# Kernel optimization log

Measured on AMD Instinct MI355X. Metric: run time of the kernel, lower is better.

The kernel has to match this reference:

```python
import jax, jax.numpy as jnp
import numpy as np

C = 256      # channels
G = 8        # groups
Cg = C // G  # channels per group (32, %16==0)
KS = 3       # kernel_size
PAD = 1
STRIDE = 1
DIL = 1
OS = 1.0     # offset_scale
DW = 3       # dw_kernel_size
Kg = KS * KS                      # sample points per group (remove_center=0)
D_OM = int(np.ceil(G * Kg * 3 / 8) * 8)  # 216, offset_mask linear out dim
N, H, W = 16, 56, 56


def setup_inputs() -> dict:
    key = jax.random.key(0)
    ks = jax.random.split(key, 8)
    inp = {}
    inp['ref'] = jax.random.normal(ks[0], (N, C, H, W), jnp.float32)
    inp['input'] = jax.random.normal(ks[1], (N, C, H, W), jnp.float32)
    inp['value_w'] = jax.random.normal(ks[2], (C, C), jnp.float32) * (1.0 / np.sqrt(C))
    inp['value_b'] = jnp.zeros((C,), jnp.float32)
    inp['dw_w'] = jax.random.normal(ks[3], (C, 2, DW, DW), jnp.float32) * 0.1
    inp['dw_b'] = jnp.zeros((C,), jnp.float32)
    # original zero-inits offset_mask; use small random weights so sampling is non-trivial
    inp['om_w'] = jax.random.normal(ks[4], (D_OM, C), jnp.float32) * 0.02
    inp['om_b'] = jnp.zeros((D_OM,), jnp.float32)
    inp['out_w'] = jax.random.normal(ks[5], (C, C), jnp.float32) * (1.0 / np.sqrt(C))
    inp['out_b'] = jnp.zeros((C,), jnp.float32)
    return inp


def _dcnv4(ref, inp, value_w, value_b, dw_w, dw_b, om_w, om_b, out_w, out_b):
    n, _, h, w = inp.shape
    # value projection on tokens (N, HW, C)
    tokens = inp.reshape(n, C, h * w).transpose(0, 2, 1)
    xv = (tokens @ value_w.T + value_b).reshape(n, h, w, G, Cg)
    # grouped depthwise-style conv on concat([input, ref]) -> offset/mask features
    cat = jnp.concatenate([inp, ref], axis=1)  # (N, 2C, H, W)
    dw = jax.lax.conv_general_dilated(
        cat, dw_w, (1, 1), ((DW // 2, DW // 2), (DW // 2, DW // 2)),
        dimension_numbers=('NCHW', 'OIHW', 'NCHW'), feature_group_count=C)
    dw = dw + dw_b[None, :, None, None]
    om = dw.transpose(0, 2, 3, 1) @ om_w.T + om_b            # (N,H,W,D_OM)
    om = om[..., :G * Kg * 3].reshape(n, h, w, G, Kg * 3)    # drop pad cols (none here)
    off = om[..., :2 * Kg].reshape(n, h, w, G, Kg, 2)        # (dx, dy) per point
    mask = om[..., 2 * Kg:]                                  # (N,H,W,G,Kg), DCNv4: no softmax
    # sampling locations (index coords): h*stride - pad + i*dil + os*dy
    ii, jj = jnp.meshgrid(jnp.arange(KS), jnp.arange(KS), indexing='ij')
    gy = (ii.reshape(-1) * DIL - PAD).astype(inp.dtype)      # (Kg,)
    gx = (jj.reshape(-1) * DIL - PAD).astype(inp.dtype)
    hh = (jnp.arange(h, dtype=inp.dtype) * STRIDE)[None, :, None, None, None]
    ww = (jnp.arange(w, dtype=inp.dtype) * STRIDE)[None, None, :, None, None]
    iy = hh + gy + OS * off[..., 1]                          # (N,H,W,G,Kg)
    ix = ww + gx + OS * off[..., 0]
    # bilinear sample with zero padding, mask-weighted sum over points
    y0 = jnp.floor(iy); x0 = jnp.floor(ix)
    fy = iy - y0; fx = ix - x0
    y0i = y0.astype(jnp.int32); x0i = x0.astype(jnp.int32)
    nidx = jnp.arange(n)[:, None, None, None, None]
    gidx = jnp.arange(G)[None, None, None, :, None]
    out = jnp.zeros((n, h, w, G, Cg), inp.dtype)
    for dy in (0, 1):
        for dx in (0, 1):
            yy = y0i + dy; xx = x0i + dx
            wgt = (fy if dy else 1.0 - fy) * (fx if dx else 1.0 - fx)
            valid = (yy >= 0) & (yy < h) & (xx >= 0) & (xx < w)
            yyc = jnp.clip(yy, 0, h - 1); xxc = jnp.clip(xx, 0, w - 1)
            gathered = xv[nidx, yyc, xxc, gidx]              # (N,H,W,G,Kg,Cg)
            out = out + jnp.einsum('nhwgp,nhwgpc->nhwgc', wgt * valid * mask, gathered)
    y = out.reshape(n, h * w, C) @ out_w.T + out_b
    return y.transpose(0, 2, 1).reshape(n, C, h, w)


def reference(ref, input, value_w, value_b, dw_w, dw_b, om_w, om_b, out_w, out_b):
    return _dcnv4(ref, input, value_w, value_b, dw_w, dw_b, om_w, om_b, out_w, out_b)
```

## Files before the change

kernel.cpp:

```cpp
#include <hip/hip_runtime.h>

#define HW 3136
#define WID 56
#define HEI 56
#define NCH 256
#define NB 16
#define MTOT (NB * HW)

typedef __attribute__((ext_vector_type(8))) short bf16x8;
typedef __attribute__((ext_vector_type(8))) unsigned short u16x8;
typedef __attribute__((ext_vector_type(4))) float f32x4;

__device__ __forceinline__ unsigned int f2bf(float f) {
    unsigned int x = __float_as_uint(f);
    return (x + 0x7fffu + ((x >> 16) & 1u)) >> 16;
}
__device__ __forceinline__ float bf2f(unsigned short u) {
    return __uint_as_float(((unsigned int)u) << 16);
}

__global__ __launch_bounds__(256) void cvt_weights(const float* __restrict__ vw,
                                                   const float* __restrict__ ow,
                                                   const float* __restrict__ outw,
                                                   unsigned short* __restrict__ dvw,
                                                   unsigned short* __restrict__ dow,
                                                   unsigned short* __restrict__ doutw) {
    int i = blockIdx.x * 256 + threadIdx.x;
    if (i < 65536) dvw[i] = (unsigned short)f2bf(vw[i]);
    else if (i < 120832) dow[i - 65536] = (unsigned short)f2bf(ow[i - 65536]);
    else if (i < 186368) doutw[i - 120832] = (unsigned short)f2bf(outw[i - 120832]);
}

template <int DOUT, int A_MODE, int OUT_MODE>
__global__ __launch_bounds__(256) void gemm_kernel(const void* __restrict__ Aptr,
                                                   const unsigned short* __restrict__ Bw,
                                                   const float* __restrict__ bias,
                                                   void* __restrict__ Out) {
    int bid = blockIdx.x;
    int nt = bid & 1;
    int mt = bid >> 1;
    int p0 = mt * 128;
    int tid = threadIdx.x;
    int lane = tid & 63;
    int wv = tid >> 6;
    int wm = wv & 1, wn = wv >> 1;
    int n0 = nt * 128;

    __shared__ __align__(16) char lds[16384 + 16384];
    char* As = lds;
    char* Bs = lds + 16384;

    int l15 = lane & 15;
    int l4 = lane >> 4;

    f32x4 acc[4][4];
    #pragma unroll
    for (int nf = 0; nf < 4; ++nf) {
        int ch = n0 + wn * 64 + nf * 16 + l15;
        float bv = (ch < DOUT) ? bias[ch] : 0.f;
        #pragma unroll
        for (int mf = 0; mf < 4; ++mf) acc[mf][nf] = (f32x4){bv, bv, bv, bv};
    }

    for (int t = 0; t < 4; ++t) {
        int k0 = t * 64;
        if (A_MODE == 0 || A_MODE == 1) {
            int px = tid & 127, kh = tid >> 7;
            unsigned int gpix = p0 + px;
            unsigned int n = gpix / HW;
            unsigned int rem = gpix - n * HW;
            #pragma unroll
            for (int h = 0; h < 4; ++h) {
                u16x8 v;
                if (A_MODE == 0) {
                    const float* src = (const float*)Aptr + ((size_t)(n * 256 + k0 + kh * 32 + h * 8)) * HW + rem;
                    #pragma unroll
                    for (int j = 0; j < 8; ++j) v[j] = (unsigned short)f2bf(src[(size_t)j * HW]);
                } else {
                    const unsigned short* src = (const unsigned short*)Aptr + ((size_t)(n * 256 + k0 + kh * 32 + h * 8)) * HW + rem;
                    #pragma unroll
                    for (int j = 0; j < 8; ++j) v[j] = src[(size_t)j * HW];
                }
                int byte = (px * 128 + (kh * 32 + h * 8) * 2) ^ ((px & 7) << 4);
                *(u16x8*)(As + byte) = v;
            }
        } else {
            int row = tid >> 1, q = tid & 1;
            const unsigned short* src = (const unsigned short*)Aptr + (size_t)(p0 + row) * 256 + k0 + q * 32;
            #pragma unroll
            for (int h = 0; h < 4; ++h) {
                u16x8 v = *(const u16x8*)(src + h * 8);
                int byte = (row * 128 + (q * 32 + h * 8) * 2) ^ ((row & 7) << 4);
                *(u16x8*)(As + byte) = v;
            }
        }
        {
            int bch = tid >> 1, kh = tid & 1;
            int ch = n0 + bch;
            bool valid = (ch < DOUT);
            const unsigned short* src = Bw + (size_t)ch * 256 + k0 + kh * 32;
            #pragma unroll
            for (int q = 0; q < 4; ++q) {
                u16x8 v = (u16x8){0, 0, 0, 0, 0, 0, 0, 0};
                if (valid) v = *(const u16x8*)(src + q * 8);
                int byte = (bch * 128 + (kh * 32 + q * 8) * 2) ^ ((bch & 7) << 4);
                *(u16x8*)(Bs + byte) = v;
            }
        }
        __syncthreads();
        bf16x8 af[4][2], bfr[4][2];
        #pragma unroll
        for (int mf = 0; mf < 4; ++mf)
            #pragma unroll
            for (int kf = 0; kf < 2; ++kf) {
                int row = wm * 64 + mf * 16 + l15;
                int byte = (row * 128 + (kf * 32 + l4 * 8) * 2) ^ ((row & 7) << 4);
                af[mf][kf] = *(bf16x8*)(As + byte);
            }
        #pragma unroll
        for (int nf = 0; nf < 4; ++nf)
            #pragma unroll
            for (int kf = 0; kf < 2; ++kf) {
                int row = wn * 64 + nf * 16 + l15;
                int byte = (row * 128 + (kf * 32 + l4 * 8) * 2) ^ ((row & 7) << 4);
                bfr[nf][kf] = *(bf16x8*)(Bs + byte);
            }
        #pragma unroll
        for (int mf = 0; mf < 4; ++mf)
            #pragma unroll
            for (int nf = 0; nf < 4; ++nf)
                #pragma unroll
                for (int kf = 0; kf < 2; ++kf)
                    acc[mf][nf] = __builtin_amdgcn_mfma_f32_16x16x32_bf16(af[mf][kf], bfr[nf][kf], acc[mf][nf], 0, 0, 0);
        __syncthreads();
    }

    #pragma unroll
    for (int mf = 0; mf < 4; ++mf) {
        int pxb = wm * 64 + mf * 16 + l4 * 4;
        unsigned int gpix = p0 + pxb;
        #pragma unroll
        for (int nf = 0; nf < 4; ++nf) {
            int ch = n0 + wn * 64 + nf * 16 + l15;
            if (OUT_MODE == 0) {
                if (ch < DOUT) {
                    float* o = (float*)Out + (size_t)gpix * DOUT + ch;
                    #pragma unroll
                    for (int j = 0; j < 4; ++j) o[(size_t)j * DOUT] = acc[mf][nf][j];
                }
            } else if (OUT_MODE == 1) {
                if (ch < DOUT) {
                    unsigned short* o = (unsigned short*)Out + (size_t)gpix * DOUT + ch;
                    #pragma unroll
                    for (int j = 0; j < 4; ++j) o[(size_t)j * DOUT] = (unsigned short)f2bf(acc[mf][nf][j]);
                }
            } else {
                unsigned int n = gpix / HW;
                unsigned int rem = gpix - n * HW;
                float* o = (float*)Out + ((size_t)(n * 256 + ch)) * HW + rem;
                *(f32x4*)o = acc[mf][nf];
            }
        }
    }
}

__global__ __launch_bounds__(256) void dwconv_kernel(const float* __restrict__ input,
                                                     const float* __restrict__ ref,
                                                     const float* __restrict__ dw_w,
                                                     const float* __restrict__ dw_b,
                                                     unsigned short* __restrict__ out) {
    int blk = blockIdx.x;
    int yt = blk % 14;
    int cb = (blk / 14) & 63;
    int n = blk / (14 * 64);
    int tid = threadIdx.x;
    int x = tid & 63;
    int c = cb * 4 + (tid >> 6);
    int y0 = yt * 4;

    const float* src = (c < 128) ? input : ref;
    int ch0 = (c < 128) ? (2 * c) : (2 * c - 256);

    float w[18];
    #pragma unroll
    for (int i = 0; i < 18; ++i) w[i] = dw_w[c * 18 + i];

    if (x < WID) {
        float bv = dw_b[c];
        float acc[4] = {bv, bv, bv, bv};
        #pragma unroll
        for (int ch = 0; ch < 2; ++ch) {
            const float* base = src + (size_t)(n * NCH + ch0 + ch) * HW;
            #pragma unroll
            for (int r = 0; r < 6; ++r) {
                int yy = y0 - 1 + r;
                bool vy = (yy >= 0) && (yy < HEI);
                const float* row = base + yy * WID;
                float lt = (vy && x > 0) ? row[x - 1] : 0.f;
                float md = vy ? row[x] : 0.f;
                float rt = (vy && x < WID - 1) ? row[x + 1] : 0.f;
                #pragma unroll
                for (int o = 0; o < 4; ++o) {
                    int ky = r - o;
                    if (ky >= 0 && ky < 3) {
                        acc[o] += lt * w[ch * 9 + ky * 3 + 0] + md * w[ch * 9 + ky * 3 + 1] + rt * w[ch * 9 + ky * 3 + 2];
                    }
                }
            }
        }
        unsigned short* o = out + (size_t)(n * NCH + c) * HW + y0 * WID + x;
        #pragma unroll
        for (int j = 0; j < 4; ++j) o[j * WID] = (unsigned short)f2bf(acc[j]);
    }
}

__global__ __launch_bounds__(256) void sample_kernel(const float* __restrict__ xv,
                                                     const unsigned short* __restrict__ om,
                                                     unsigned short* __restrict__ sout) {
    int blk = blockIdx.x;
    int n = blk / (HW / 16);
    int p0 = (blk % (HW / 16)) * 16;
    int tid = threadIdx.x;

    __shared__ __align__(16) float swt[1152][4];
    __shared__ __align__(8) ushort soff[1152][4];

    for (int i = tid; i < 1152; i += 256) {
        int pix = i / 72;
        int r = i % 72;
        int g = r / 9;
        int pt = r % 9;
        int glob = p0 + pix;
        int py = glob / WID, px = glob % WID;
        const unsigned short* ob = om + ((size_t)n * HW + glob) * 216 + g * 27;
        float ox = bf2f(ob[2 * pt]);
        float oy = bf2f(ob[2 * pt + 1]);
        float m = bf2f(ob[18 + pt]);
        float iy = (float)(py + pt / 3 - 1) + oy;
        float ix = (float)(px + pt % 3 - 1) + ox;
        float fy0 = floorf(iy), fx0 = floorf(ix);
        float fy = iy - fy0, fx = ix - fx0;
        int y0 = (int)fy0, x0 = (int)fx0;
        #pragma unroll
        for (int dy = 0; dy < 2; ++dy) {
            #pragma unroll
            for (int dx = 0; dx < 2; ++dx) {
                int yy = y0 + dy, xx = x0 + dx;
                bool valid = (yy >= 0) & (yy < HEI) & (xx >= 0) & (xx < WID);
                int yc = min(max(yy, 0), HEI - 1);
                int xc = min(max(xx, 0), WID - 1);
                float wv = (dy ? fy : 1.f - fy) * (dx ? fx : 1.f - fx) * m;
                swt[i][dy * 2 + dx] = valid ? wv : 0.f;
                soff[i][dy * 2 + dx] = (ushort)(yc * WID + xc);
            }
        }
    }
    __syncthreads();

    int pix = tid >> 4;
    int t16 = tid & 15;
    const float* xvb = xv + (size_t)n * HW * 256;
    unsigned short* so = sout + ((size_t)n * HW + p0 + pix) * 256;

    #pragma unroll
    for (int i = 0; i < 2; ++i) {
        int chunk = t16 + 16 * i;
        int g = chunk >> 2, c8 = chunk & 3;
        int widx = pix * 72 + g * 9;
        const float* xc = xvb + g * 32 + c8 * 8;
        f32x4 a0 = (f32x4){0.f, 0.f, 0.f, 0.f};
        f32x4 a1 = (f32x4){0.f, 0.f, 0.f, 0.f};
        #pragma unroll
        for (int pt = 0; pt < 9; ++pt) {
            float4 w = *(const float4*)&swt[widx + pt][0];
            ushort4 o = *(const ushort4*)&soff[widx + pt][0];
            const float* s0 = xc + (size_t)o.x * 256;
            const float* s1 = xc + (size_t)o.y * 256;
            const float* s2 = xc + (size_t)o.z * 256;
            const float* s3 = xc + (size_t)o.w * 256;
            f32x4 w0 = (f32x4){w.x, w.x, w.x, w.x};
            f32x4 w1 = (f32x4){w.y, w.y, w.y, w.y};
            f32x4 w2 = (f32x4){w.z, w.z, w.z, w.z};
            f32x4 w3 = (f32x4){w.w, w.w, w.w, w.w};
            a0 += w0 * *(const f32x4*)(s0) + w1 * *(const f32x4*)(s1) + w2 * *(const f32x4*)(s2) + w3 * *(const f32x4*)(s3);
            a1 += w0 * *(const f32x4*)(s0 + 4) + w1 * *(const f32x4*)(s1 + 4) + w2 * *(const f32x4*)(s2 + 4) + w3 * *(const f32x4*)(s3 + 4);
        }
        u16x8 st;
        #pragma unroll
        for (int j = 0; j < 4; ++j) st[j] = (unsigned short)f2bf(a0[j]);
        #pragma unroll
        for (int j = 0; j < 4; ++j) st[4 + j] = (unsigned short)f2bf(a1[j]);
        *(u16x8*)(so + g * 32 + c8 * 8) = st;
    }
}

extern "C" void kernel_launch(void* const* d_in, const int* in_sizes, int n_in,
                              void* d_out, int out_size, void* d_ws, size_t ws_size,
                              hipStream_t stream) {
    const float* ref     = (const float*)d_in[0];
    const float* input   = (const float*)d_in[1];
    const float* value_w = (const float*)d_in[2];
    const float* value_b = (const float*)d_in[3];
    const float* dw_w    = (const float*)d_in[4];
    const float* dw_b    = (const float*)d_in[5];
    const float* om_w    = (const float*)d_in[6];
    const float* om_b    = (const float*)d_in[7];
    const float* out_w   = (const float*)d_in[8];
    const float* out_b   = (const float*)d_in[9];
    float* out = (float*)d_out;

    char* ws = (char*)d_ws;
    float* xv            = (float*)ws;
    unsigned short* dwb  = (unsigned short*)(ws + (size_t)MTOT * 256 * 4);
    unsigned short* sout = (unsigned short*)(ws + (size_t)MTOT * 256 * 6);
    unsigned short* omb  = (unsigned short*)(ws + (size_t)MTOT * 256 * 8);
    char* wbase          = ws + (size_t)MTOT * 256 * 8 + (size_t)MTOT * 216 * 2;
    unsigned short* vw_bf   = (unsigned short*)(wbase);
    unsigned short* ow_bf   = (unsigned short*)(wbase + 131072);
    unsigned short* outw_bf = (unsigned short*)(wbase + 131072 + 110592);

    cvt_weights<<<728, 256, 0, stream>>>(value_w, om_w, out_w, vw_bf, ow_bf, outw_bf);
    gemm_kernel<256, 0, 0><<<(MTOT / 128) * 2, 256, 0, stream>>>(input, vw_bf, value_b, xv);
    dwconv_kernel<<<NB * 64 * 14, 256, 0, stream>>>(input, ref, dw_w, dw_b, dwb);
    gemm_kernel<216, 1, 1><<<(MTOT / 128) * 2, 256, 0, stream>>>(dwb, ow_bf, om_b, omb);
    sample_kernel<<<NB * (HW / 16), 256, 0, stream>>>(xv, omb, sout);
    gemm_kernel<256, 2, 2><<<(MTOT / 128) * 2, 256, 0, stream>>>(sout, outw_bf, out_b, out);
}
```

Measured before the change: 330.7 us.

## Load full-K A tile once per block and store value projection in bf16

The GEMM kernel now stages the whole 128x256 A tile in LDS once and loops over both 128-column N tiles inside the block. Previously each N tile was a separate block that re-read A from global memory. The value projection output xv is now written as bf16 rather than fp32, so the sampling kernel gathers half as many bytes and converts on load. The cost is 80KB of dynamic LDS per block, which limits occupancy, plus extra bf16 rounding of the sampled values.

Measured after the change: 277.7 us. -16.0%, faster.

```diff
diff --git a/kernel.cpp b/kernel.cpp
--- a/kernel.cpp
+++ b/kernel.cpp
@@ -32,133 +32,133 @@
 }
 
 template <int DOUT, int A_MODE, int OUT_MODE>
-__global__ __launch_bounds__(256) void gemm_kernel(const void* __restrict__ Aptr,
-                                                   const unsigned short* __restrict__ Bw,
-                                                   const float* __restrict__ bias,
-                                                   void* __restrict__ Out) {
-    int bid = blockIdx.x;
-    int nt = bid & 1;
-    int mt = bid >> 1;
-    int p0 = mt * 128;
+__global__ __launch_bounds__(256, 2) void gemm_kernel(const void* __restrict__ Aptr,
+                                                      const unsigned short* __restrict__ Bw,
+                                                      const float* __restrict__ bias,
+                                                      void* __restrict__ Out) {
+    int p0 = blockIdx.x * 128;
     int tid = threadIdx.x;
     int lane = tid & 63;
     int wv = tid >> 6;
     int wm = wv & 1, wn = wv >> 1;
-    int n0 = nt * 128;
-
-    __shared__ __align__(16) char lds[16384 + 16384];
-    char* As = lds;
-    char* Bs = lds + 16384;
-
     int l15 = lane & 15;
     int l4 = lane >> 4;
 
-    f32x4 acc[4][4];
+    extern __shared__ __align__(16) char lds[];
+    char* As = lds;
+    char* Bs = lds + 65536;
+
+    if (A_MODE == 0 || A_MODE == 1) {
+        int px = tid & 127, khalf = tid >> 7;
+        unsigned int gpix = p0 + px;
+        unsigned int n = gpix / HW;
+        unsigned int rem = gpix - n * HW;
+        #pragma unroll
+        for (int h = 0; h < 16; ++h) {
+            int k = khalf * 128 + h * 8;
+            u16x8 v;
+            if (A_MODE == 0) {
+                const float* src = (const float*)Aptr + ((size_t)(n * 256 + k)) * HW + rem;
+                #pragma unroll
+                for (int j = 0; j < 8; ++j) v[j] = (unsigned short)f2bf(src[(size_t)j * HW]);
+            } else {
+                const unsigned short* src = (const unsigned short*)Aptr + ((size_t)(n * 256 + k)) * HW + rem;
+                #pragma unroll
+                for (int j = 0; j < 8; ++j) v[j] = src[(size_t)j * HW];
+            }
+            int byte = px * 512 + ((k * 2) ^ ((px & 7) << 4));
+            *(u16x8*)(As + byte) = v;
+        }
+    } else {
+        int row = tid >> 1, khalf = tid & 1;
+        const unsigned short* src = (const unsigned short*)Aptr + (size_t)(p0 + row) * 256 + khalf * 128;
+        #pragma unroll
+        for (int h = 0; h < 16; ++h) {
+            u16x8 v = *(const u16x8*)(src + h * 8);
+            int k2 = (khalf * 128 + h * 8) * 2;
+            int byte = row * 512 + (k2 ^ ((row & 7) << 4));
+            *(u16x8*)(As + byte) = v;
+        }
+    }
+
     #pragma unroll
-    for (int nf = 0; nf < 4; ++nf) {
-        int ch = n0 + wn * 64 + nf * 16 + l15;
-        float bv = (ch < DOUT) ? bias[ch] : 0.f;
-        #pragma unroll
-        for (int mf = 0; mf < 4; ++mf) acc[mf][nf] = (f32x4){bv, bv, bv, bv};
-    }
-
-    for (int t = 0; t < 4; ++t) {
-        int k0 = t * 64;
-        if (A_MODE == 0 || A_MODE == 1) {
-            int px = tid & 127, kh = tid >> 7;
-            unsigned int gpix = p0 + px;
-            unsigned int n = gpix / HW;
-            unsigned int rem = gpix - n * HW;
-            #pragma unroll
-            for (int h = 0; h < 4; ++h) {
-                u16x8 v;
-                if (A_MODE == 0) {
-                    const float* src = (const float*)Aptr + ((size_t)(n * 256 + k0 + kh * 32 + h * 8)) * HW + rem;
-                    #pragma unroll
-                    for (int j = 0; j < 8; ++j) v[j] = (unsigned short)f2bf(src[(size_t)j * HW]);
-                } else {
-                    const unsigned short* src = (const unsigned short*)Aptr + ((size_t)(n * 256 + k0 + kh * 32 + h * 8)) * HW + rem;
-                    #pragma unroll
-                    for (int j = 0; j < 8; ++j) v[j] = src[(size_t)j * HW];
-                }
-                int byte = (px * 128 + (kh * 32 + h * 8) * 2) ^ ((px & 7) << 4);
-                *(u16x8*)(As + byte) = v;
-            }
-        } else {
-            int row = tid >> 1, q = tid & 1;
-            const unsigned short* src = (const unsigned short*)Aptr + (size_t)(p0 + row) * 256 + k0 + q * 32;
-            #pragma unroll
-            for (int h = 0; h < 4; ++h) {
-                u16x8 v = *(const u16x8*)(src + h * 8);
-                int byte = (row * 128 + (q * 32 + h * 8) * 2) ^ ((row & 7) << 4);
-                *(u16x8*)(As + byte) = v;
-            }
-        }
-        {
-            int bch = tid >> 1, kh = tid & 1;
-            int ch = n0 + bch;
-            bool valid = (ch < DOUT);
-            const unsigned short* src = Bw + (size_t)ch * 256 + k0 + kh * 32;
-            #pragma unroll
-            for (int q = 0; q < 4; ++q) {
-                u16x8 v = (u16x8){0, 0, 0, 0, 0, 0, 0, 0};
-                if (valid) v = *(const u16x8*)(src + q * 8);
-                int byte = (bch * 128 + (kh * 32 + q * 8) * 2) ^ ((bch & 7) << 4);
-                *(u16x8*)(Bs + byte) = v;
-            }
-        }
-        __syncthreads();
-        bf16x8 af[4][2], bfr[4][2];
-        #pragma unroll
-        for (int mf = 0; mf < 4; ++mf)
-            #pragma unroll
-            for (int kf = 0; kf < 2; ++kf) {
-                int row = wm * 64 + mf * 16 + l15;
-                int byte = (row * 128 + (kf * 32 + l4 * 8) * 2) ^ ((row & 7) << 4);
-                af[mf][kf] = *(bf16x8*)(As + byte);
-            }
-        #pragma unroll
-        for (int nf = 0; nf < 4; ++nf)
-            #pragma unroll
-            for (int kf = 0; kf < 2; ++kf) {
-                int row = wn * 64 + nf * 16 + l15;
-                int byte = (row * 128 + (kf * 32 + l4 * 8) * 2) ^ ((row & 7) << 4);
-                bfr[nf][kf] = *(bf16x8*)(Bs + byte);
-            }
-        #pragma unroll
-        for (int mf = 0; mf < 4; ++mf)
-            #pragma unroll
-            for (int nf = 0; nf < 4; ++nf)
-                #pragma unroll
-                for (int kf = 0; kf < 2; ++kf)
-                    acc[mf][nf] = __builtin_amdgcn_mfma_f32_16x16x32_bf16(af[mf][kf], bfr[nf][kf], acc[mf][nf], 0, 0, 0);
-        __syncthreads();
-    }
-
-    #pragma unroll
-    for (int mf = 0; mf < 4; ++mf) {
-        int pxb = wm * 64 + mf * 16 + l4 * 4;
-        unsigned int gpix = p0 + pxb;
+    for (int nt = 0; nt < 2; ++nt) {
+        int n0 = nt * 128;
+
+        f32x4 acc[4][4];
         #pragma unroll
         for (int nf = 0; nf < 4; ++nf) {
             int ch = n0 + wn * 64 + nf * 16 + l15;
-            if (OUT_MODE == 0) {
-                if (ch < DOUT) {
-                    float* o = (float*)Out + (size_t)gpix * DOUT + ch;
+            float bv = (DOUT == 256 || ch < DOUT) ? bias[ch] : 0.f;
+            #pragma unroll
+            for (int mf = 0; mf < 4; ++mf) acc[mf][nf] = (f32x4){bv, bv, bv, bv};
+        }
+
+        for (int t = 0; t < 4; ++t) {
+            int k0 = t * 64;
+            __syncthreads();
+            {
+                int bch = tid >> 1, kh = tid & 1;
+                int ch = n0 + bch;
+                bool valid = (DOUT == 256) || (ch < DOUT);
+                const unsigned short* src = Bw + (size_t)ch * 256 + k0 + kh * 32;
+                #pragma unroll
+                for (int q = 0; q < 4; ++q) {
+                    u16x8 v = (u16x8){0, 0, 0, 0, 0, 0, 0, 0};
+                    if (valid) v = *(const u16x8*)(src + q * 8);
+                    int k2 = (kh * 32 + q * 8) * 2;
+                    int byte = bch * 128 + (k2 ^ ((bch & 7) << 4));
+                    *(u16x8*)(Bs + byte) = v;
+                }
+            }
+            __syncthreads();
+            bf16x8 af[4][2], bfr[4][2];
+            #pragma unroll
+            for (int mf = 0; mf < 4; ++mf)
+                #pragma unroll
+                for (int kf = 0; kf < 2; ++kf) {
+                    int row = wm * 64 + mf * 16 + l15;
+                    int k2 = (k0 + kf * 32 + l4 * 8) * 2;
+                    int byte = row * 512 + (k2 ^ ((row & 7) << 4));
+                    af[mf][kf] = *(bf16x8*)(As + byte);
+                }
+            #pragma unroll
+            for (int nf = 0; nf < 4; ++nf)
+                #pragma unroll
+                for (int kf = 0; kf < 2; ++kf) {
+                    int row = wn * 64 + nf * 16 + l15;
+                    int k2 = (kf * 32 + l4 * 8) * 2;
+                    int byte = row * 128 + (k2 ^ ((row & 7) << 4));
+                    bfr[nf][kf] = *(bf16x8*)(Bs + byte);
+                }
+            #pragma unroll
+            for (int mf = 0; mf < 4; ++mf)
+                #pragma unroll
+                for (int nf = 0; nf < 4; ++nf)
                     #pragma unroll
-                    for (int j = 0; j < 4; ++j) o[(size_t)j * DOUT] = acc[mf][nf][j];
-                }
-            } else if (OUT_MODE == 1) {
-                if (ch < DOUT) {
-                    unsigned short* o = (unsigned short*)Out + (size_t)gpix * DOUT + ch;
-                    #pragma unroll
-                    for (int j = 0; j < 4; ++j) o[(size_t)j * DOUT] = (unsigned short)f2bf(acc[mf][nf][j]);
-                }
-            } else {
-                unsigned int n = gpix / HW;
-                unsigned int rem = gpix - n * HW;
-                float* o = (float*)Out + ((size_t)(n * 256 + ch)) * HW + rem;
-                *(f32x4*)o = acc[mf][nf];
+                    for (int kf = 0; kf < 2; ++kf)
+                        acc[mf][nf] = __builtin_amdgcn_mfma_f32_16x16x32_bf16(af[mf][kf], bfr[nf][kf], acc[mf][nf], 0, 0, 0);
+        }
+
+        #pragma unroll
+        for (int mf = 0; mf < 4; ++mf) {
+            int pxb = wm * 64 + mf * 16 + l4 * 4;
+            unsigned int gpix = p0 + pxb;
+            #pragma unroll
+            for (int nf = 0; nf < 4; ++nf) {
+                int ch = n0 + wn * 64 + nf * 16 + l15;
+                if (OUT_MODE == 1) {
+                    if (DOUT == 256 || ch < DOUT) {
+                        unsigned short* o = (unsigned short*)Out + (size_t)gpix * DOUT + ch;
+                        #pragma unroll
+                        for (int j = 0; j < 4; ++j) o[(size_t)j * DOUT] = (unsigned short)f2bf(acc[mf][nf][j]);
+                    }
+                } else {
+                    unsigned int n = gpix / HW;
+                    unsigned int rem = gpix - n * HW;
+                    float* o = (float*)Out + ((size_t)(n * 256 + ch)) * HW + rem;
+                    *(f32x4*)o = acc[mf][nf];
+                }
             }
         }
     }
@@ -214,7 +214,7 @@
     }
 }
 
-__global__ __launch_bounds__(256) void sample_kernel(const float* __restrict__ xv,
+__global__ __launch_bounds__(256) void sample_kernel(const unsigned short* __restrict__ xv,
                                                      const unsigned short* __restrict__ om,
                                                      unsigned short* __restrict__ sout) {
     int blk = blockIdx.x;
@@ -259,7 +259,7 @@
 
     int pix = tid >> 4;
     int t16 = tid & 15;
-    const float* xvb = xv + (size_t)n * HW * 256;
+    const unsigned short* xvb = xv + (size_t)n * HW * 256;
     unsigned short* so = sout + ((size_t)n * HW + p0 + pix) * 256;
 
     #pragma unroll
@@ -267,29 +267,26 @@
         int chunk = t16 + 16 * i;
         int g = chunk >> 2, c8 = chunk & 3;
         int widx = pix * 72 + g * 9;
-        const float* xc = xvb + g * 32 + c8 * 8;
-        f32x4 a0 = (f32x4){0.f, 0.f, 0.f, 0.f};
-        f32x4 a1 = (f32x4){0.f, 0.f, 0.f, 0.f};
+        const unsigned short* xc = xvb + g * 32 + c8 * 8;
+        float acc[8];
+        #pragma unroll
+        for (int j = 0; j < 8; ++j) acc[j] = 0.f;
         #pragma unroll
         for (int pt = 0; pt < 9; ++pt) {
             float4 w = *(const float4*)&swt[widx + pt][0];
             ushort4 o = *(const ushort4*)&soff[widx + pt][0];
-            const float* s0 = xc + (size_t)o.x * 256;
-            const float* s1 = xc + (size_t)o.y * 256;
-            const float* s2 = xc + (size_t)o.z * 256;
-            const float* s3 = xc + (size_t)o.w * 256;
-            f32x4 w0 = (f32x4){w.x, w.x, w.x, w.x};
-            f32x4 w1 = (f32x4){w.y, w.y, w.y, w.y};
-            f32x4 w2 = (f32x4){w.z, w.z, w.z, w.z};
-            f32x4 w3 = (f32x4){w.w, w.w, w.w, w.w};
-            a0 += w0 * *(const f32x4*)(s0) + w1 * *(const f32x4*)(s1) + w2 * *(const f32x4*)(s2) + w3 * *(const f32x4*)(s3);
-            a1 += w0 * *(const f32x4*)(s0 + 4) + w1 * *(const f32x4*)(s1 + 4) + w2 * *(const f32x4*)(s2 + 4) + w3 * *(const f32x4*)(s3 + 4);
+            u16x8 r0 = *(const u16x8*)(xc + (size_t)o.x * 256);
+            u16x8 r1 = *(const u16x8*)(xc + (size_t)o.y * 256);
+            u16x8 r2 = *(const u16x8*)(xc + (size_t)o.z * 256);
+            u16x8 r3 = *(const u16x8*)(xc + (size_t)o.w * 256);
+            #pragma unroll
+            for (int j = 0; j < 8; ++j) {
+                acc[j] += w.x * bf2f(r0[j]) + w.y * bf2f(r1[j]) + w.z * bf2f(r2[j]) + w.w * bf2f(r3[j]);
+            }
         }
         u16x8 st;
         #pragma unroll
-        for (int j = 0; j < 4; ++j) st[j] = (unsigned short)f2bf(a0[j]);
-        #pragma unroll
-        for (int j = 0; j < 4; ++j) st[4 + j] = (unsigned short)f2bf(a1[j]);
+        for (int j = 0; j < 8; ++j) st[j] = (unsigned short)f2bf(acc[j]);
         *(u16x8*)(so + g * 32 + c8 * 8) = st;
     }
 }
@@ -310,19 +307,22 @@
     float* out = (float*)d_out;
 
     char* ws = (char*)d_ws;
-    float* xv            = (float*)ws;
-    unsigned short* dwb  = (unsigned short*)(ws + (size_t)MTOT * 256 * 4);
-    unsigned short* sout = (unsigned short*)(ws + (size_t)MTOT * 256 * 6);
-    unsigned short* omb  = (unsigned short*)(ws + (size_t)MTOT * 256 * 8);
-    char* wbase          = ws + (size_t)MTOT * 256 * 8 + (size_t)MTOT * 216 * 2;
+    const size_t BF = (size_t)MTOT * 256 * 2;
+    unsigned short* xv   = (unsigned short*)(ws);
+    unsigned short* dwb  = (unsigned short*)(ws + BF);
+    unsigned short* sout = (unsigned short*)(ws + 2 * BF);
+    unsigned short* omb  = (unsigned short*)(ws + 3 * BF);
+    char* wbase          = ws + 3 * BF + (size_t)MTOT * 216 * 2;
     unsigned short* vw_bf   = (unsigned short*)(wbase);
     unsigned short* ow_bf   = (unsigned short*)(wbase + 131072);
     unsigned short* outw_bf = (unsigned short*)(wbase + 131072 + 110592);
 
+    const size_t GEMM_LDS = 65536 + 16384;
+
     cvt_weights<<<728, 256, 0, stream>>>(value_w, om_w, out_w, vw_bf, ow_bf, outw_bf);
-    gemm_kernel<256, 0, 0><<<(MTOT / 128) * 2, 256, 0, stream>>>(input, vw_bf, value_b, xv);
+    gemm_kernel<256, 0, 1><<<MTOT / 128, 256, GEMM_LDS, stream>>>(input, vw_bf, value_b, xv);
     dwconv_kernel<<<NB * 64 * 14, 256, 0, stream>>>(input, ref, dw_w, dw_b, dwb);
-    gemm_kernel<216, 1, 1><<<(MTOT / 128) * 2, 256, 0, stream>>>(dwb, ow_bf, om_b, omb);
+    gemm_kernel<216, 1, 1><<<MTOT / 128, 256, GEMM_LDS, stream>>>(dwb, ow_bf, om_b, omb);
     sample_kernel<<<NB * (HW / 16), 256, 0, stream>>>(xv, omb, sout);
-    gemm_kernel<256, 2, 2><<<(MTOT / 128) * 2, 256, 0, stream>>>(sout, outw_bf, out_b, out);
-}
+    gemm_kernel<256, 2, 2><<<MTOT / 128, 256, GEMM_LDS, stream>>>(sout, outw_bf, out_b, out);
+}
```
